# Performance work log

Measured on AMD Instinct MI355X. Metric: run time of the kernel, lower is better.

## Reference

```python
import jax, jax.numpy as jnp
import numpy as np

N_NODES = 50000
N_EDGES = 800000
N_FEAT = 16
N_BASIS = 4
GAMMA = 10.0
R_MAX = 5.0
INV_SQRT2 = 0.7071067811865476


def setup_inputs() -> dict:
    key = jax.random.key(0)
    k1, k2, k3, k4 = jax.random.split(key, 4)
    pos = jax.random.normal(k1, (N_NODES, 3), dtype=jnp.float32)
    node_features = jax.random.normal(k2, (N_NODES, N_FEAT), dtype=jnp.float32)
    # build edges with no self-loops: dst = (src + 1 + r) % N, r in [0, N-2]
    src = jax.random.randint(k3, (N_EDGES,), 0, N_NODES)
    r = jax.random.randint(k4, (N_EDGES,), 0, N_NODES - 1)
    dst = (src + 1 + r) % N_NODES
    edge_idx = jnp.stack([src, dst], axis=0).astype(jnp.int64)
    return {"pos": pos, "node_features": node_features, "edge_idx": edge_idx}


def _gaussian_basis(d):
    # d: [E] -> [E, N_BASIS]
    centers = jnp.linspace(0.0, R_MAX, N_BASIS, dtype=d.dtype)
    return jnp.exp(-GAMMA * (d[:, None] - centers[None, :]) ** 2)


def _pos_to_rep(v):
    # v: [N, 3, C] cartesian along axis -2 -> complex spherical l=1 basis,
    # returned as stacked (real, imag): [2, N, 3, C]
    x, y, z = v[..., 0, :], v[..., 1, :], v[..., 2, :]
    zero = jnp.zeros_like(z)
    real = jnp.stack([x * INV_SQRT2, z, -x * INV_SQRT2], axis=-2)
    imag = jnp.stack([-y * INV_SQRT2, zero, -y * INV_SQRT2], axis=-2)
    return jnp.stack([real, imag], axis=0)


def reference(pos, node_features, edge_idx):
    src, dst = edge_idx[0], edge_idx[1]
    disp = pos[dst] - pos[src]                      # [E, 3]
    dist = jnp.linalg.norm(disp, axis=-1)           # [E]
    bf = _gaussian_basis(dist)                      # [E, B]
    unit = disp / dist[:, None]                     # [E, 3]
    nf = node_features[dst]                         # [E, F]
    # outer products: [E, 3, B, F]
    edge_vals = (unit[:, :, None, None] * bf[:, None, :, None]
                 * nf[:, None, None, :])
    edge_vals = edge_vals.reshape(edge_vals.shape[0], 3, N_BASIS * N_FEAT)
    node_vecs = jax.ops.segment_sum(edge_vals, src, num_segments=N_NODES)  # [N,3,C]
    return _pos_to_rep(node_vecs)
```

## Files before the change

kernel.cpp:

```cpp
#include <hip/hip_runtime.h>

#define N_FEAT 16
#define N_BASIS 4
#define GAMMA 10.0f
#define R_MAX 5.0f
#define INV_SQRT2 0.70710678118654752f

#define BUCKET 64
#define CAP 1360
#define MAXB 1024
#define SC_BLOCK 512
#define SC_EDGES 4096
#define ACC_BLOCK 512

#define KC      (-GAMMA * 1.4426950408889634f)
#define CKD     (R_MAX / (N_BASIS - 1))

#if __has_builtin(__builtin_amdgcn_exp2f)
#define EXP2(x) __builtin_amdgcn_exp2f(x)
#else
#define EXP2(x) exp2f(x)
#endif

__global__ void bucket_scatter_kernel(const int* __restrict__ src,
                                      const int* __restrict__ dst,
                                      const float* __restrict__ pos,
                                      float4* __restrict__ pos4,
                                      int* __restrict__ gcursor,
                                      int* __restrict__ sorted,
                                      int n_edges, int nbuck, int n_nodes) {
    __shared__ int h[MAXB];
    __shared__ int cur[MAXB];
    __shared__ int gbase[MAXB];
    __shared__ int pay[SC_EDGES];

    int t = threadIdx.x;

    {
        int i = blockIdx.x * SC_BLOCK + t;
        if (i < n_nodes)
            pos4[i] = make_float4(pos[3 * i], pos[3 * i + 1], pos[3 * i + 2], 0.0f);
    }

    int base_e = blockIdx.x * SC_EDGES;
    int nloc = n_edges - base_e;
    if (nloc > SC_EDGES) nloc = SC_EDGES;

    for (int i = t; i < nbuck; i += SC_BLOCK) h[i] = 0;
    __syncthreads();

    unsigned pk[8];
    bool ok[8];
#pragma unroll
    for (int r = 0; r < 8; ++r) {
        int i = t + r * SC_BLOCK;
        ok[r] = (i < nloc);
        unsigned s = ok[r] ? (unsigned)src[base_e + i] : 0u;
        unsigned d = ok[r] ? (unsigned)dst[base_e + i] : 0u;
        pk[r] = (s << 16) | d;
        if (ok[r]) atomicAdd(&h[s >> 6], 1);
    }
    __syncthreads();

    if (t < 64) {
        int run = 0;
        for (int base = 0; base < nbuck; base += 64) {
            int i = base + t;
            int v = (i < nbuck) ? h[i] : 0;
            int incl = v;
            for (int off = 1; off < 64; off <<= 1) {
                int y = __shfl_up(incl, off, 64);
                if (t >= off) incl += y;
            }
            if (i < nbuck) h[i] = run + incl - v;
            run += __shfl(incl, 63, 64);
        }
    }
    __syncthreads();
    for (int i = t; i < nbuck; i += SC_BLOCK) cur[i] = h[i];
    __syncthreads();

#pragma unroll
    for (int r = 0; r < 8; ++r) {
        if (ok[r]) {
            int b = (int)(pk[r] >> 22);
            int p = atomicAdd(&cur[b], 1);
            pay[p] = (int)pk[r];
        }
    }
    __syncthreads();

    for (int b = t; b < nbuck; b += SC_BLOCK) {
        int c = cur[b] - h[b];
        gbase[b] = (c > 0) ? atomicAdd(&gcursor[b], c) : 0;
    }
    __syncthreads();

    for (int i = t; i < nloc; i += SC_BLOCK) {
        unsigned P = (unsigned)pay[i];
        int b = (int)(P >> 22);
        int idx = gbase[b] + (i - h[b]);
        if (idx < CAP) sorted[b * CAP + idx] = (int)P;
    }
}

__global__ __launch_bounds__(ACC_BLOCK) void accumulate_kernel(
        const float4* __restrict__ pos4,
        const float* __restrict__ nfeat,
        const int* __restrict__ sorted,
        const int* __restrict__ gcursor,
        float* __restrict__ out,
        int n_nodes) {
    __shared__ int spay[CAP + 64];
    __shared__ int off[BUCKET + 1];
    __shared__ int cnt[BUCKET];
    __shared__ int cur[BUCKET];
    __shared__ float4 spos[BUCKET];

    int b = blockIdx.x;
    int t = threadIdx.x;
    int w = t >> 6;
    int lane = t & 63;
    int grp = lane >> 4;
    int f = lane & 15;
    int nbase = b << 6;

    int ecnt = gcursor[b];
    if (ecnt > CAP) ecnt = CAP;
    const int* seg = sorted + b * CAP;

    if (t < BUCKET) {
        cnt[t] = 0;
        int gn = nbase + t;
        spos[t] = (gn < n_nodes) ? pos4[gn] : make_float4(0.f, 0.f, 0.f, 0.f);
    }
    __syncthreads();

    for (int i = t; i < ecnt; i += ACC_BLOCK)
        atomicAdd(&cnt[((unsigned)seg[i] >> 16) & 63], 1);
    __syncthreads();

    if (t < 64) {
        int v = cnt[t];
        int incl = v;
        for (int o2 = 1; o2 < 64; o2 <<= 1) {
            int y = __shfl_up(incl, o2, 64);
            if (t >= o2) incl += y;
        }
        off[t + 1] = incl;
        if (t == 0) off[0] = 0;
        cur[t] = incl - v;
    }
    __syncthreads();

    for (int i = t; i < ecnt; i += ACC_BLOCK) {
        int E = seg[i];
        int p = atomicAdd(&cur[((unsigned)E >> 16) & 63], 1);
        spay[p] = E;
    }
    __syncthreads();

    for (int set = 0; set < 2; ++set) {
        int nl = (w << 3) + (set << 2) + grp;
        int gn = nbase + nl;
        int myoff = off[nl];
        int deg = off[nl + 1] - myoff;
        float4 ps = spos[nl];

        int m1 = max(deg, __shfl_xor(deg, 16, 64));
        int maxdeg = max(m1, __shfl_xor(m1, 32, 64));

        float ax0 = 0.f, ax1 = 0.f, ax2 = 0.f, ax3 = 0.f;
        float ay0 = 0.f, ay1 = 0.f, ay2 = 0.f, ay3 = 0.f;
        float az0 = 0.f, az1 = 0.f, az2 = 0.f, az3 = 0.f;

        if (maxdeg > 0) {
            int degm1 = (deg > 0) ? deg - 1 : 0;
            int E1;
            float4 p0;
            float nf0;
            {
                int i0 = myoff + 0;
                int E0 = spay[i0];
                E1 = spay[myoff + min(1, degm1)];
                int d0 = (deg > 0) ? (E0 & 0xFFFF) : 0;
                p0 = pos4[d0];
                nf0 = nfeat[(d0 << 4) + f];
            }
            for (int s = 0; s < maxdeg; ++s) {
                bool clv = (s < deg);
                float4 cp = p0;
                float cnf = nf0;

                int E2 = spay[myoff + min(s + 2, degm1)];
                int d1 = ((s + 1) < deg) ? (E1 & 0xFFFF) : 0;
                p0 = pos4[d1];
                nf0 = nfeat[(d1 << 4) + f];
                E1 = E2;

                float dx = cp.x - ps.x, dy = cp.y - ps.y, dz = cp.z - ps.z;
                float r2 = dx * dx + dy * dy + dz * dz;
                r2 = clv ? r2 : 1.0f;
                float inv = __builtin_amdgcn_rsqf(r2);
                float dist = r2 * inv;
                float nfi = clv ? cnf * inv : 0.0f;
                float q = dist * dist * KC;
#define KSTEP(KK, AX, AY, AZ)                                          \
                {                                                      \
                    const float ck = (float)(KK) * CKD;                \
                    const float mk = -2.0f * KC * ck;                  \
                    const float qk = KC * ck * ck;                     \
                    float bb = EXP2(fmaf(dist, mk, q + qk));           \
                    float val = bb * nfi;                              \
                    AX = fmaf(dx, val, AX);                            \
                    AY = fmaf(dy, val, AY);                            \
                    AZ = fmaf(dz, val, AZ);                            \
                }
                KSTEP(0, ax0, ay0, az0);
                KSTEP(1, ax1, ay1, az1);
                KSTEP(2, ax2, ay2, az2);
                KSTEP(3, ax3, ay3, az3);
#undef KSTEP
            }
        }

        if (gn < n_nodes) {
            float* re = out + (size_t)gn * 192;
            float* im = out + (size_t)n_nodes * 192 + (size_t)gn * 192;
#define WOUT(KK, AX, AY, AZ)                                           \
            {                                                          \
                int o1 = (KK) * 16 + f;                                \
                float xs = (AX)*INV_SQRT2;                             \
                float ys = -(AY)*INV_SQRT2;                            \
                re[o1]       = xs;                                     \
                re[64 + o1]  = (AZ);                                   \
                re[128 + o1] = -xs;                                    \
                im[o1]       = ys;                                     \
                im[64 + o1]  = 0.0f;                                   \
                im[128 + o1] = ys;                                     \
            }
            WOUT(0, ax0, ay0, az0);
            WOUT(1, ax1, ay1, az1);
            WOUT(2, ax2, ay2, az2);
            WOUT(3, ax3, ay3, az3);
#undef WOUT
        }
    }
}

extern "C" void kernel_launch(void* const* d_in, const int* in_sizes, int n_in,
                              void* d_out, int out_size, void* d_ws, size_t ws_size,
                              hipStream_t stream) {
    const float* pos = (const float*)d_in[0];
    const float* nfeat = (const float*)d_in[1];
    const int* edge_idx = (const int*)d_in[2];

    int n_nodes = in_sizes[0] / 3;
    int n_edges = in_sizes[2] / 2;

    const int* src = edge_idx;
    const int* dst = edge_idx + n_edges;

    float* out = (float*)d_out;
    int nbuck = (n_nodes + 63) >> 6;

    char* ws = (char*)d_ws;
    size_t o = 0;
    auto alloc = [&](size_t bytes) {
        char* p = ws + o;
        o = (o + bytes + 255) & ~(size_t)255;
        return p;
    };
    int* gcursor = (int*)alloc((size_t)nbuck * 4);
    int* sorted  = (int*)alloc((size_t)nbuck * CAP * 4);
    float4* pos4 = (float4*)alloc((size_t)n_nodes * 16);

    hipMemsetAsync(gcursor, 0, (size_t)nbuck * sizeof(int), stream);

    {
        int grid = (n_edges + SC_EDGES - 1) / SC_EDGES;
        bucket_scatter_kernel<<<grid, SC_BLOCK, 0, stream>>>(src, dst, pos, pos4,
                                                             gcursor, sorted,
                                                             n_edges, nbuck, n_nodes);
    }

    accumulate_kernel<<<nbuck, ACC_BLOCK, 0, stream>>>(pos4, nfeat, sorted, gcursor,
                                                       out, n_nodes);
}
```

Before: 63.89 us.

## Compute per-node edge outer-product sums with fp16 MFMA matrix instructions

```diff
diff --git a/kernel.cpp b/kernel.cpp
--- a/kernel.cpp
+++ b/kernel.cpp
@@ -13,6 +13,9 @@
 #define SC_EDGES 4096
 #define ACC_BLOCK 512
 
+#define SLOTCAP 2560
+#define ROWSTRIDE 2568
+
 #define KC      (-GAMMA * 1.4426950408889634f)
 #define CKD     (R_MAX / (N_BASIS - 1))
 
@@ -21,6 +24,9 @@
 #else
 #define EXP2(x) exp2f(x)
 #endif
+
+typedef _Float16 half8 __attribute__((ext_vector_type(8)));
+typedef float f32x4 __attribute__((ext_vector_type(4)));
 
 __global__ void bucket_scatter_kernel(const int* __restrict__ src,
                                       const int* __restrict__ dst,
@@ -111,17 +117,18 @@
         const int* __restrict__ gcursor,
         float* __restrict__ out,
         int n_nodes) {
-    __shared__ int spay[CAP + 64];
-    __shared__ int off[BUCKET + 1];
-    __shared__ int cnt[BUCKET];
-    __shared__ int cur[BUCKET];
-    __shared__ float4 spos[BUCKET];
+    __shared__ _Float16 a_lds[12 * ROWSTRIDE];
+    __shared__ unsigned short slot_dst[SLOTCAP];
+    __shared__ int cnt[64];
+    __shared__ int soff[64];
+    __shared__ int curs[64];
+    __shared__ float4 spos[64];
 
     int b = blockIdx.x;
     int t = threadIdx.x;
     int w = t >> 6;
     int lane = t & 63;
-    int grp = lane >> 4;
+    int q = lane >> 4;
     int f = lane & 15;
     int nbase = b << 6;
 
@@ -129,7 +136,14 @@
     if (ecnt > CAP) ecnt = CAP;
     const int* seg = sorted + b * CAP;
 
-    if (t < BUCKET) {
+    {
+        int4 z4 = make_int4(0, 0, 0, 0);
+        int4* az = (int4*)a_lds;
+        for (int i = t; i < 3852; i += ACC_BLOCK) az[i] = z4;
+        int4* sz = (int4*)slot_dst;
+        for (int i = t; i < 320; i += ACC_BLOCK) sz[i] = z4;
+    }
+    if (t < 64) {
         cnt[t] = 0;
         int gn = nbase + t;
         spos[t] = (gn < n_nodes) ? pos4[gn] : make_float4(0.f, 0.f, 0.f, 0.f);
@@ -141,109 +155,88 @@
     __syncthreads();
 
     if (t < 64) {
-        int v = cnt[t];
-        int incl = v;
+        int deg = cnt[t];
+        int pad = (deg + 31) & ~31;
+        int incl = pad;
         for (int o2 = 1; o2 < 64; o2 <<= 1) {
             int y = __shfl_up(incl, o2, 64);
             if (t >= o2) incl += y;
         }
-        off[t + 1] = incl;
-        if (t == 0) off[0] = 0;
-        cur[t] = incl - v;
+        int excl = incl - pad;
+        soff[t] = excl;
+        curs[t] = excl;
     }
     __syncthreads();
 
     for (int i = t; i < ecnt; i += ACC_BLOCK) {
-        int E = seg[i];
-        int p = atomicAdd(&cur[((unsigned)E >> 16) & 63], 1);
-        spay[p] = E;
-    }
-    __syncthreads();
-
-    for (int set = 0; set < 2; ++set) {
-        int nl = (w << 3) + (set << 2) + grp;
+        unsigned E = (unsigned)seg[i];
+        int d = E & 0xFFFF;
+        int sl = (E >> 16) & 63;
+        int p = atomicAdd(&curs[sl], 1);
+        if (p < SLOTCAP) {
+            float4 pd = pos4[d];
+            float4 ps = spos[sl];
+            float dx = pd.x - ps.x, dy = pd.y - ps.y, dz = pd.z - ps.z;
+            float r2 = dx * dx + dy * dy + dz * dz;
+            float inv = __builtin_amdgcn_rsqf(r2);
+            float dist = r2 * inv;
+            float ux = dx * inv, uy = dy * inv, uz = dz * inv;
+            slot_dst[p] = (unsigned short)d;
+#pragma unroll
+            for (int kk = 0; kk < N_BASIS; ++kk) {
+                float ck = (float)kk * CKD;
+                float tt = dist - ck;
+                float bb = EXP2(tt * tt * KC);
+                a_lds[(kk)*ROWSTRIDE + p]      = (_Float16)(ux * bb);
+                a_lds[(4 + kk)*ROWSTRIDE + p]  = (_Float16)(uy * bb);
+                a_lds[(8 + kk)*ROWSTRIDE + p]  = (_Float16)(uz * bb);
+            }
+        }
+    }
+    __syncthreads();
+
+    int arow = (f < 12) ? f : 11;
+    for (int nl = w; nl < 64; nl += ACC_BLOCK / 64) {
+        int deg = cnt[nl];
+        int base = soff[nl];
+        int ntiles = (deg + 31) >> 5;
+        int maxt = (SLOTCAP - base) >> 5;
+        if (ntiles > maxt) ntiles = maxt;
+
+        f32x4 C = {0.f, 0.f, 0.f, 0.f};
+        for (int tile = 0; tile < ntiles; ++tile) {
+            int k0 = base + (tile << 5) + (q << 3);
+            half8 a = *(const half8*)&a_lds[arow * ROWSTRIDE + k0];
+            const unsigned short* dp = &slot_dst[k0];
+            half8 bf;
+#pragma unroll
+            for (int j = 0; j < 8; ++j)
+                bf[j] = (_Float16)nfeat[((int)dp[j] << 4) + f];
+            C = __builtin_amdgcn_mfma_f32_16x16x32_f16(a, bf, C, 0, 0, 0);
+        }
+
         int gn = nbase + nl;
-        int myoff = off[nl];
-        int deg = off[nl + 1] - myoff;
-        float4 ps = spos[nl];
-
-        int m1 = max(deg, __shfl_xor(deg, 16, 64));
-        int maxdeg = max(m1, __shfl_xor(m1, 32, 64));
-
-        float ax0 = 0.f, ax1 = 0.f, ax2 = 0.f, ax3 = 0.f;
-        float ay0 = 0.f, ay1 = 0.f, ay2 = 0.f, ay3 = 0.f;
-        float az0 = 0.f, az1 = 0.f, az2 = 0.f, az3 = 0.f;
-
-        if (maxdeg > 0) {
-            int degm1 = (deg > 0) ? deg - 1 : 0;
-            int E1;
-            float4 p0;
-            float nf0;
-            {
-                int i0 = myoff + 0;
-                int E0 = spay[i0];
-                E1 = spay[myoff + min(1, degm1)];
-                int d0 = (deg > 0) ? (E0 & 0xFFFF) : 0;
-                p0 = pos4[d0];
-                nf0 = nfeat[(d0 << 4) + f];
-            }
-            for (int s = 0; s < maxdeg; ++s) {
-                bool clv = (s < deg);
-                float4 cp = p0;
-                float cnf = nf0;
-
-                int E2 = spay[myoff + min(s + 2, degm1)];
-                int d1 = ((s + 1) < deg) ? (E1 & 0xFFFF) : 0;
-                p0 = pos4[d1];
-                nf0 = nfeat[(d1 << 4) + f];
-                E1 = E2;
-
-                float dx = cp.x - ps.x, dy = cp.y - ps.y, dz = cp.z - ps.z;
-                float r2 = dx * dx + dy * dy + dz * dz;
-                r2 = clv ? r2 : 1.0f;
-                float inv = __builtin_amdgcn_rsqf(r2);
-                float dist = r2 * inv;
-                float nfi = clv ? cnf * inv : 0.0f;
-                float q = dist * dist * KC;
-#define KSTEP(KK, AX, AY, AZ)                                          \
-                {                                                      \
-                    const float ck = (float)(KK) * CKD;                \
-                    const float mk = -2.0f * KC * ck;                  \
-                    const float qk = KC * ck * ck;                     \
-                    float bb = EXP2(fmaf(dist, mk, q + qk));           \
-                    float val = bb * nfi;                              \
-                    AX = fmaf(dx, val, AX);                            \
-                    AY = fmaf(dy, val, AY);                            \
-                    AZ = fmaf(dz, val, AZ);                            \
-                }
-                KSTEP(0, ax0, ay0, az0);
-                KSTEP(1, ax1, ay1, az1);
-                KSTEP(2, ax2, ay2, az2);
-                KSTEP(3, ax3, ay3, az3);
-#undef KSTEP
-            }
-        }
-
         if (gn < n_nodes) {
             float* re = out + (size_t)gn * 192;
-            float* im = out + (size_t)n_nodes * 192 + (size_t)gn * 192;
-#define WOUT(KK, AX, AY, AZ)                                           \
-            {                                                          \
-                int o1 = (KK) * 16 + f;                                \
-                float xs = (AX)*INV_SQRT2;                             \
-                float ys = -(AY)*INV_SQRT2;                            \
-                re[o1]       = xs;                                     \
-                re[64 + o1]  = (AZ);                                   \
-                re[128 + o1] = -xs;                                    \
-                im[o1]       = ys;                                     \
-                im[64 + o1]  = 0.0f;                                   \
-                im[128 + o1] = ys;                                     \
+            float* im = re + (size_t)n_nodes * 192;
+#pragma unroll
+            for (int r = 0; r < 4; ++r) {
+                float v = C[r];
+                int o1 = r * 16 + f;
+                if (q == 0) {
+                    float xs = v * INV_SQRT2;
+                    re[o1] = xs;
+                    re[128 + o1] = -xs;
+                } else if (q == 1) {
+                    float ys = -v * INV_SQRT2;
+                    im[o1] = ys;
+                    im[128 + o1] = ys;
+                } else if (q == 2) {
+                    re[64 + o1] = v;
+                } else {
+                    im[64 + o1] = 0.0f;
+                }
             }
-            WOUT(0, ax0, ay0, az0);
-            WOUT(1, ax1, ay1, az1);
-            WOUT(2, ax2, ay2, az2);
-            WOUT(3, ax3, ay3, az3);
-#undef WOUT
         }
     }
 }
```

Result: faster. 61.57 us (-3.6%).
